# Optimization experiments

Hardware: AMD Instinct MI355X
Metric: run time of the kernel (lower is better)

Reference implementation:

```python
import jax, jax.numpy as jnp
import numpy as np

VOCAB, T, IN, H, L = 32000, 4096, 512, 256, 2


def setup_inputs() -> dict:
    key = jax.random.key(0)
    ks = jax.random.split(key, 32)
    inp = {}
    inp["tokens"] = jax.random.randint(ks[0], (T,), 0, VOCAB)
    inp["emb"] = jax.random.normal(ks[1], (VOCAB, IN), dtype=jnp.float32) * 0.02
    i = 2
    for d in ("f", "b"):
        for l in range(L):
            in_l = IN if l == 0 else H
            inp[f"{d}_Wih{l}"] = jax.random.normal(ks[i], (4 * H, in_l), dtype=jnp.float32) * 0.05; i += 1
            inp[f"{d}_Whh{l}"] = jax.random.normal(ks[i], (4 * H, H), dtype=jnp.float32) * 0.05; i += 1
            inp[f"{d}_bih{l}"] = jnp.zeros((4 * H,), dtype=jnp.float32)
            inp[f"{d}_bhh{l}"] = jnp.zeros((4 * H,), dtype=jnp.float32)
    return inp


def _lstm_layer(x_seq, Wih, Whh, bih, bhh):
    # x_seq: [T, in]; torch.nn.LSTMCell gate order: i, f, g, o
    Hh = Whh.shape[1]
    b = bih + bhh
    def step(carry, x):
        h, c = carry
        g = x @ Wih.T + h @ Whh.T + b           # [4H]
        i_, f_, g_, o_ = jnp.split(g, 4)
        c = jax.nn.sigmoid(f_) * c + jax.nn.sigmoid(i_) * jnp.tanh(g_)
        h = jax.nn.sigmoid(o_) * jnp.tanh(c)
        return (h, c), h
    z = jnp.zeros((Hh,), x_seq.dtype)
    (h, c), hs = jax.lax.scan(step, (z, z), x_seq)
    return hs, h, c                              # [T,H], [H], [H]


def _run_dir(x_seq, params):
    finals = []
    h_seq = x_seq
    for (Wih, Whh, bih, bhh) in params:
        h_seq, h, c = _lstm_layer(h_seq, Wih, Whh, bih, bhh)
        finals.append((c, h))
    return h_seq, finals


def reference(tokens, emb,
              f_Wih0, f_Whh0, f_bih0, f_bhh0, f_Wih1, f_Whh1, f_bih1, f_bhh1,
              b_Wih0, b_Whh0, b_bih0, b_bhh0, b_Wih1, b_Whh1, b_bih1, b_bhh1):
    x = emb[tokens]                              # [T, IN] embedding lookup
    fparams = [(f_Wih0, f_Whh0, f_bih0, f_bhh0), (f_Wih1, f_Whh1, f_bih1, f_bhh1)]
    bparams = [(b_Wih0, b_Whh0, b_bih0, b_bhh0), (b_Wih1, b_Whh1, b_bih1, b_bhh1)]
    f_out, f_fin = _run_dir(x, fparams)          # forward over sequence
    b_out_rev, b_fin = _run_dir(x[::-1], bparams)  # backward over reversed sequence
    b_out = b_out_rev[::-1]
    outputs = jnp.concatenate([f_out, b_out], axis=-1)  # [T, 2H]
    cell_memories = jnp.stack([jnp.stack([f_fin[l][0], b_fin[l][0]]) for l in range(L)])  # [L,2,H]
    hidden_states = jnp.stack([jnp.stack([f_fin[l][1], b_fin[l][1]]) for l in range(L)])  # [L,2,H]
    return cell_memories, hidden_states, outputs
```

## Files before the change

### kernel.cpp

```cpp
#include <hip/hip_runtime.h>
#include <math.h>

#define T_SEQ 4096

__device__ __forceinline__ float sigmoidf_(float x) {
  return 1.0f / (1.0f + expf(-x));
}

__device__ __forceinline__ unsigned long long pack_h(int tag, float h) {
  return ((unsigned long long)(unsigned)tag << 32) |
         (unsigned long long)__float_as_uint(h);
}

__device__ __forceinline__ unsigned long long ld_mall(const unsigned long long* p) {
  unsigned long long v;
  asm volatile("global_load_dwordx2 %0, %1, off sc0 sc1\n\ts_waitcnt vmcnt(0)"
               : "=v"(v) : "v"(p) : "memory");
  return v;
}
__device__ __forceinline__ void st_mall(unsigned long long* p, unsigned long long v) {
  asm volatile("global_store_dwordx2 %0, %1, off sc0 sc1"
               :: "v"(p), "v"(v) : "memory");
}
__device__ __forceinline__ float poll_mall(const unsigned long long* p, unsigned want) {
  for (;;) {
    unsigned long long v = ld_mall(p);
    if ((unsigned)(v >> 32) == want) return __uint_as_float((unsigned)v);
  }
}

__device__ __forceinline__ void bar() {
  asm volatile("s_waitcnt lgkmcnt(0)" ::: "memory");
  __builtin_amdgcn_s_barrier();
  asm volatile("" ::: "memory");
}

#define DECL_W8(p) float4 p##0, p##1, p##2, p##3, p##4, p##5, p##6, p##7
#define LOAD_W8(p, src) do { const float4* _s = (const float4*)(src); \
  p##0=_s[0]; p##1=_s[1]; p##2=_s[2]; p##3=_s[3]; \
  p##4=_s[4]; p##5=_s[5]; p##6=_s[6]; p##7=_s[7]; } while (0)
#define PIN4(v4) asm volatile("" : "+v"((v4).x), "+v"((v4).y), \
                                   "+v"((v4).z), "+v"((v4).w))
#define PIN_W8(p) do { PIN4(p##0); PIN4(p##1); PIN4(p##2); PIN4(p##3); \
  PIN4(p##4); PIN4(p##5); PIN4(p##6); PIN4(p##7); } while (0)
#define FMA4(acc, W_, H_) do { acc = fmaf((W_).x, (H_).x, acc); \
  acc = fmaf((W_).y, (H_).y, acc); acc = fmaf((W_).z, (H_).z, acc); \
  acc = fmaf((W_).w, (H_).w, acc); } while (0)

__global__ void gather_emb(const int* __restrict__ tokens,
                           const float4* __restrict__ emb4,
                           float4* __restrict__ X4) {
  int i = blockIdx.x * 256 + threadIdx.x;
  int t = i >> 7;
  int q = i & 127;
  X4[i] = emb4[(long)tokens[t] * 128 + q];
}

__global__ __launch_bounds__(256) void gemm_proj(
    const float* __restrict__ Xf, const float* __restrict__ Xb, int revb,
    const float* __restrict__ Wf, const float* __restrict__ Wb,
    const float* __restrict__ bihf, const float* __restrict__ bhhf,
    const float* __restrict__ bihb, const float* __restrict__ bhhb,
    float* __restrict__ Pf, float* __restrict__ Pb, int K)
{
  const int dirb = blockIdx.z;
  const float* X  = dirb ? Xb : Xf;
  const float* W  = dirb ? Wb : Wf;
  const float* bih = dirb ? bihb : bihf;
  const float* bhh = dirb ? bhhb : bhhf;
  float* Pp = dirb ? Pb : Pf;
  const int rev = dirb ? revb : 0;

  const int bn = blockIdx.x;
  const int bm = blockIdx.y;
  const int tid = threadIdx.x;
  const int tx = tid & 15, ty = tid >> 4;

  __shared__ float Xs[16][68];
  __shared__ float Ws[16][68];

  float acc[4][4] = {{0.f}};

  const int lrow = tid >> 2;
  const int lk4  = (tid & 3) * 4;
  const int xrow = bm * 64 + lrow;
  const int xsrc = rev ? (4095 - xrow) : xrow;
  const float* xptr = X + (long)xsrc * K + lk4;
  const float* wptr = W + (long)(bn * 64 + lrow) * K + lk4;

  for (int k0 = 0; k0 < K; k0 += 16) {
    float4 xv = *(const float4*)(xptr + k0);
    float4 wv = *(const float4*)(wptr + k0);
    __syncthreads();
    Xs[lk4 + 0][lrow] = xv.x; Xs[lk4 + 1][lrow] = xv.y;
    Xs[lk4 + 2][lrow] = xv.z; Xs[lk4 + 3][lrow] = xv.w;
    Ws[lk4 + 0][lrow] = wv.x; Ws[lk4 + 1][lrow] = wv.y;
    Ws[lk4 + 2][lrow] = wv.z; Ws[lk4 + 3][lrow] = wv.w;
    __syncthreads();
    #pragma unroll
    for (int kk = 0; kk < 16; ++kk) {
      float4 a = *(const float4*)(&Xs[kk][ty * 4]);
      float4 b = *(const float4*)(&Ws[kk][tx * 4]);
      acc[0][0] = fmaf(a.x, b.x, acc[0][0]); acc[0][1] = fmaf(a.x, b.y, acc[0][1]);
      acc[0][2] = fmaf(a.x, b.z, acc[0][2]); acc[0][3] = fmaf(a.x, b.w, acc[0][3]);
      acc[1][0] = fmaf(a.y, b.x, acc[1][0]); acc[1][1] = fmaf(a.y, b.y, acc[1][1]);
      acc[1][2] = fmaf(a.y, b.z, acc[1][2]); acc[1][3] = fmaf(a.y, b.w, acc[1][3]);
      acc[2][0] = fmaf(a.z, b.x, acc[2][0]); acc[2][1] = fmaf(a.z, b.y, acc[2][1]);
      acc[2][2] = fmaf(a.z, b.z, acc[2][2]); acc[2][3] = fmaf(a.z, b.w, acc[2][3]);
      acc[3][0] = fmaf(a.w, b.x, acc[3][0]); acc[3][1] = fmaf(a.w, b.y, acc[3][1]);
      acc[3][2] = fmaf(a.w, b.z, acc[3][2]); acc[3][3] = fmaf(a.w, b.w, acc[3][3]);
    }
  }

  const int c0 = bn * 64 + tx * 4;
  #pragma unroll
  for (int i = 0; i < 4; ++i) {
    const int r = bm * 64 + ty * 4 + i;
    float4 o4;
    o4.x = acc[i][0] + bih[c0 + 0] + bhh[c0 + 0];
    o4.y = acc[i][1] + bih[c0 + 1] + bhh[c0 + 1];
    o4.z = acc[i][2] + bih[c0 + 2] + bhh[c0 + 2];
    o4.w = acc[i][3] + bih[c0 + 3] + bhh[c0 + 3];
    *(float4*)(&Pp[(long)r * 1024 + c0]) = o4;
  }
}

__global__ __launch_bounds__(512, 1) void lstm_fused(
    const float* __restrict__ P0f, const float* __restrict__ P0b,
    const float* __restrict__ Whh0f, const float* __restrict__ Whh0b,
    const float* __restrict__ Wih1f, const float* __restrict__ Whh1f,
    const float* __restrict__ bih1f, const float* __restrict__ bhh1f,
    const float* __restrict__ Wih1b, const float* __restrict__ Whh1b,
    const float* __restrict__ bih1b, const float* __restrict__ bhh1b,
    float* __restrict__ out,
    unsigned long long* __restrict__ ring0,
    unsigned long long* __restrict__ h1x)
{
  const int bx = blockIdx.x;
  const int t  = threadIdx.x;
  const int d   = bx & 1;
  const int sub = bx >> 1;

  __shared__ float hx[512];
  __shared__ float part[8 * 264];

  unsigned long long* ring = ring0 + (long)d * T_SEQ * 256;

  if (sub < 4) {
    const int w = sub;
    const int wbase = w * 64;
    const float* __restrict__ P = d ? P0b : P0f;
    const float* __restrict__ W = d ? Whh0b : Whh0f;

    const int kb = t >> 6;
    const int jg = t & 63;

    DECL_W8(wa); DECL_W8(wb); DECL_W8(wc); DECL_W8(wd);
    LOAD_W8(wa, W + (long)(0 * 256 + wbase + jg) * 256 + kb * 32);
    LOAD_W8(wb, W + (long)(1 * 256 + wbase + jg) * 256 + kb * 32);
    LOAD_W8(wc, W + (long)(2 * 256 + wbase + jg) * 256 + kb * 32);
    LOAD_W8(wd, W + (long)(3 * 256 + wbase + jg) * 256 + kb * 32);
    PIN_W8(wa); PIN_W8(wb); PIN_W8(wc); PIN_W8(wd);

    const long pj = (long)((t & 3) * 256 + wbase + (t >> 2));

    float pv_cur = 0.0f, c_prev = 0.0f;
    if (t < 256) { pv_cur = P[pj]; hx[t] = 0.0f; }

    for (int s = 0; s < T_SEQ; ++s) {
      if (s > 0 && t >= 256 && t < 448) {
        const int q = t - 256;
        const int pcell = (q < wbase) ? q : q + 64;
        hx[pcell] = poll_mall(ring + (long)(s - 1) * 256 + pcell, (unsigned)s);
      }
      float pv_next = 0.0f;
      if (t < 256 && s + 1 < T_SEQ) pv_next = P[(long)(s + 1) * 1024 + pj];
      bar();

      float a0 = 0.f, a1 = 0.f, a2 = 0.f, a3 = 0.f;
      const float4* h4 = (const float4*)&hx[kb * 32];
      #define L0STEP(q) do { float4 hv = h4[q]; FMA4(a0, wa##q, hv); \
        FMA4(a1, wb##q, hv); FMA4(a2, wc##q, hv); FMA4(a3, wd##q, hv); } while (0)
      L0STEP(0); L0STEP(1); L0STEP(2); L0STEP(3);
      L0STEP(4); L0STEP(5); L0STEP(6); L0STEP(7);
      #undef L0STEP
      float4 av; av.x = a0; av.y = a1; av.z = a2; av.w = a3;
      *(float4*)(&part[kb * 264 + jg * 4]) = av;
      bar();

      if (t < 256) {
        float g = pv_cur;
        #pragma unroll
        for (int q = 0; q < 8; ++q) g += part[q * 264 + t];
        float act = ((t & 3) == 2) ? tanhf(g) : sigmoidf_(g);
        float y  = __shfl_xor(act, 1);
        float zx = __shfl_xor(act, 2);
        float zy = __shfl_xor(y, 2);
        const bool l1b = (t & 1), h1b = (t & 2);
        float i_ = h1b ? (l1b ? zy : zx) : (l1b ? y : act);
        float f_ = h1b ? (l1b ? zx : zy) : (l1b ? act : y);
        float g_ = h1b ? (l1b ? y : act) : (l1b ? zy : zx);
        float o_ = h1b ? (l1b ? act : y) : (l1b ? zx : zy);
        float c = f_ * c_prev + i_ * g_;
        c_prev = c;
        float h = o_ * tanhf(c);
        pv_cur = pv_next;
        if ((t & 3) == 0) {
          const int gc = wbase + (t >> 2);
          hx[gc] = h;
          st_mall(ring + (long)s * 256 + gc, pack_h(s + 1, h));
          if (s == T_SEQ - 1) {
            out[d * 256 + gc] = c;
            out[1024 + d * 256 + gc] = h;
          }
        }
      }
    }
  } else {
    const int w1 = sub - 4;
    const int wbase1 = w1 * 32;
    const float* __restrict__ Wih = d ? Wih1b : Wih1f;
    const float* __restrict__ Whh = d ? Whh1b : Whh1f;
    const float* __restrict__ bih = d ? bih1b : bih1f;
    const float* __restrict__ bhh = d ? bhh1b : bhh1f;
    unsigned long long* slot = h1x + d * 512;
    float* hout = d ? (out + 2048 + (long)4095 * 512 + 256) : (out + 2048);
    const long hstr = d ? -512 : 512;

    const int kb = t >> 6;
    const int jg = t & 63;

    const int m0 = jg * 2, m1 = m0 + 1;
    const int j0 = (m0 & 3) * 256 + wbase1 + (m0 >> 2);
    const int j1 = (m1 & 3) * 256 + wbase1 + (m1 >> 2);
    const float* s0 = (kb < 4) ? (Wih + (long)j0 * 256 + kb * 64)
                               : (Whh + (long)j0 * 256 + (kb - 4) * 64);
    const float* s1 = (kb < 4) ? (Wih + (long)j1 * 256 + kb * 64)
                               : (Whh + (long)j1 * 256 + (kb - 4) * 64);
    DECL_W8(ua); DECL_W8(ub); DECL_W8(uc); DECL_W8(ud);
    LOAD_W8(ua, s0); LOAD_W8(ub, s0 + 32);
    LOAD_W8(uc, s1); LOAD_W8(ud, s1 + 32);
    PIN_W8(ua); PIN_W8(ub); PIN_W8(uc); PIN_W8(ud);

    float bsum = 0.0f, c_prev = 0.0f;
    if (t < 128) {
      const int j = (t & 3) * 256 + wbase1 + (t >> 2);
      bsum = bih[j] + bhh[j];
      if ((t & 3) == 0) hx[256 + wbase1 + (t >> 2)] = 0.0f;
    }

    for (int s = 0; s < T_SEQ; ++s) {
      if (t >= 128 && t < 384) {
        const int c0_ = t - 128;
        hx[c0_] = poll_mall(ring + (long)s * 256 + c0_, (unsigned)(s + 1));
      } else {
        int q1 = -1;
        if (t < 128) { if ((t & 3) != 0) q1 = (t >> 2) * 3 + (t & 3) - 1; }
        else q1 = 96 + (t - 384);
        if (q1 >= 0) {
          const int pc1 = (q1 < wbase1) ? q1 : q1 + 32;
          hx[256 + pc1] = poll_mall(slot + ((s + 1) & 1) * 256 + pc1,
                                    (unsigned)s);
        }
      }
      bar();

      float a0 = 0.f, a1 = 0.f;
      const float4* h4 = (const float4*)&hx[kb * 64];
      #define L1STEPA(q) do { float4 hv = h4[q];     FMA4(a0, ua##q, hv); \
        FMA4(a1, uc##q, hv); } while (0)
      #define L1STEPB(q) do { float4 hv = h4[8 + q]; FMA4(a0, ub##q, hv); \
        FMA4(a1, ud##q, hv); } while (0)
      L1STEPA(0); L1STEPA(1); L1STEPA(2); L1STEPA(3);
      L1STEPA(4); L1STEPA(5); L1STEPA(6); L1STEPA(7);
      L1STEPB(0); L1STEPB(1); L1STEPB(2); L1STEPB(3);
      L1STEPB(4); L1STEPB(5); L1STEPB(6); L1STEPB(7);
      #undef L1STEPA
      #undef L1STEPB
      float2 av2; av2.x = a0; av2.y = a1;
      *(float2*)(&part[kb * 264 + jg * 2]) = av2;
      bar();

      if (t < 128) {
        float g = bsum;
        #pragma unroll
        for (int q = 0; q < 8; ++q) g += part[q * 264 + t];
        float act = ((t & 3) == 2) ? tanhf(g) : sigmoidf_(g);
        float y  = __shfl_xor(act, 1);
        float zx = __shfl_xor(act, 2);
        float zy = __shfl_xor(y, 2);
        const bool l1b = (t & 1), h1b = (t & 2);
        float i_ = h1b ? (l1b ? zy : zx) : (l1b ? y : act);
        float f_ = h1b ? (l1b ? zx : zy) : (l1b ? act : y);
        float g_ = h1b ? (l1b ? y : act) : (l1b ? zy : zx);
        float o_ = h1b ? (l1b ? act : y) : (l1b ? zx : zy);
        float c = f_ * c_prev + i_ * g_;
        c_prev = c;
        float h = o_ * tanhf(c);
        if ((t & 3) == 0) {
          const int gc = wbase1 + (t >> 2);
          hx[256 + gc] = h;
          st_mall(&slot[(s & 1) * 256 + gc], pack_h(s + 1, h));
          hout[(long)s * hstr + gc] = h;
          if (s == T_SEQ - 1) {
            out[512 + d * 256 + gc] = c;
            out[1024 + 512 + d * 256 + gc] = h;
          }
        }
      }
    }
  }
}

extern "C" void kernel_launch(void* const* d_in, const int* in_sizes, int n_in,
                              void* d_out, int out_size, void* d_ws, size_t ws_size,
                              hipStream_t stream) {
  const int*   tokens = (const int*)d_in[0];
  const float* emb    = (const float*)d_in[1];
  const float* fWih0 = (const float*)d_in[2];
  const float* fWhh0 = (const float*)d_in[3];
  const float* fbih0 = (const float*)d_in[4];
  const float* fbhh0 = (const float*)d_in[5];
  const float* fWih1 = (const float*)d_in[6];
  const float* fWhh1 = (const float*)d_in[7];
  const float* fbih1 = (const float*)d_in[8];
  const float* fbhh1 = (const float*)d_in[9];
  const float* bWih0 = (const float*)d_in[10];
  const float* bWhh0 = (const float*)d_in[11];
  const float* bbih0 = (const float*)d_in[12];
  const float* bbhh0 = (const float*)d_in[13];
  const float* bWih1 = (const float*)d_in[14];
  const float* bWhh1 = (const float*)d_in[15];
  const float* bbih1 = (const float*)d_in[16];
  const float* bbhh1 = (const float*)d_in[17];

  float* out = (float*)d_out;
  float* ws  = (float*)d_ws;

  float* X   = ws;
  float* P0f = ws + 4194304;
  float* P0b = ws + 8388608;
  unsigned long long* ring0 = (unsigned long long*)ws;
  unsigned long long* h1x   = (unsigned long long*)(ws + 12582912);

  gather_emb<<<2048, 256, 0, stream>>>(tokens, (const float4*)emb, (float4*)X);

  gemm_proj<<<dim3(16, 64, 2), 256, 0, stream>>>(
      X, X, 1, fWih0, bWih0, fbih0, fbhh0, bbih0, bbhh0, P0f, P0b, 512);

  hipMemsetAsync(ring0, 0, (size_t)2 * T_SEQ * 256 * sizeof(unsigned long long), stream);
  hipMemsetAsync(h1x, 0, 1024 * sizeof(unsigned long long), stream);

  lstm_fused<<<dim3(24), 512, 0, stream>>>(
      P0f, P0b, fWhh0, bWhh0,
      fWih1, fWhh1, fbih1, fbhh1,
      bWih1, bWhh1, bbih1, bbhh1,
      out, ring0, h1x);
}
```

Measured before the change: 7.064 ms.

## Replace LDS partial-sum reduction with lane shuffles and double-buffer hidden state

Remaps the threads of each recurrent block so that the lanes sharing one gate row split the K dimension, and combines their partial dot products with xor shuffles instead of writing them to shared memory. This removes the second barrier per timestep. The hidden-state buffer is double-buffered in shared memory so that the next step's writes cannot race with the current step's reads. Cross-block flag loads and stores switch from cache-bypassing inline asm to atomicOr and atomicExch, which may raise the latency of each poll.

Result: slower. 12.16 ms (+72.2%).

```diff
diff --git a/kernel.cpp b/kernel.cpp
--- a/kernel.cpp
+++ b/kernel.cpp
@@ -12,19 +12,12 @@
          (unsigned long long)__float_as_uint(h);
 }
 
-__device__ __forceinline__ unsigned long long ld_mall(const unsigned long long* p) {
-  unsigned long long v;
-  asm volatile("global_load_dwordx2 %0, %1, off sc0 sc1\n\ts_waitcnt vmcnt(0)"
-               : "=v"(v) : "v"(p) : "memory");
-  return v;
-}
-__device__ __forceinline__ void st_mall(unsigned long long* p, unsigned long long v) {
-  asm volatile("global_store_dwordx2 %0, %1, off sc0 sc1"
-               :: "v"(p), "v"(v) : "memory");
-}
-__device__ __forceinline__ float poll_mall(const unsigned long long* p, unsigned want) {
+__device__ __forceinline__ void st_a(unsigned long long* p, unsigned long long v) {
+  atomicExch(p, v);
+}
+__device__ __forceinline__ float poll_a(unsigned long long* p, unsigned want) {
   for (;;) {
-    unsigned long long v = ld_mall(p);
+    unsigned long long v = atomicOr(p, 0ull);
     if ((unsigned)(v >> 32) == want) return __uint_as_float((unsigned)v);
   }
 }
@@ -46,6 +39,16 @@
 #define FMA4(acc, W_, H_) do { acc = fmaf((W_).x, (H_).x, acc); \
   acc = fmaf((W_).y, (H_).y, acc); acc = fmaf((W_).z, (H_).z, acc); \
   acc = fmaf((W_).w, (H_).w, acc); } while (0)
+#define G8(acc, p, off) do { \
+  { float4 hv = h4[off + 0]; FMA4(acc, p##0, hv); } \
+  { float4 hv = h4[off + 1]; FMA4(acc, p##1, hv); } \
+  { float4 hv = h4[off + 2]; FMA4(acc, p##2, hv); } \
+  { float4 hv = h4[off + 3]; FMA4(acc, p##3, hv); } \
+  { float4 hv = h4[off + 4]; FMA4(acc, p##4, hv); } \
+  { float4 hv = h4[off + 5]; FMA4(acc, p##5, hv); } \
+  { float4 hv = h4[off + 6]; FMA4(acc, p##6, hv); } \
+  { float4 hv = h4[off + 7]; FMA4(acc, p##7, hv); } \
+} while (0)
 
 __global__ void gather_emb(const int* __restrict__ tokens,
                            const float4* __restrict__ emb4,
@@ -141,8 +144,7 @@
   const int d   = bx & 1;
   const int sub = bx >> 1;
 
-  __shared__ float hx[512];
-  __shared__ float part[8 * 264];
+  __shared__ float hx2[2][512];
 
   unsigned long long* ring = ring0 + (long)d * T_SEQ * 256;
 
@@ -152,67 +154,55 @@
     const float* __restrict__ P = d ? P0b : P0f;
     const float* __restrict__ W = d ? Whh0b : Whh0f;
 
-    const int kb = t >> 6;
-    const int jg = t & 63;
+    const int cell = t >> 3, gate = (t >> 1) & 3, kh = t & 1;
+    const int j = gate * 256 + wbase + cell;
 
     DECL_W8(wa); DECL_W8(wb); DECL_W8(wc); DECL_W8(wd);
-    LOAD_W8(wa, W + (long)(0 * 256 + wbase + jg) * 256 + kb * 32);
-    LOAD_W8(wb, W + (long)(1 * 256 + wbase + jg) * 256 + kb * 32);
-    LOAD_W8(wc, W + (long)(2 * 256 + wbase + jg) * 256 + kb * 32);
-    LOAD_W8(wd, W + (long)(3 * 256 + wbase + jg) * 256 + kb * 32);
+    const float* wsrc = W + (long)j * 256 + kh * 128;
+    LOAD_W8(wa, wsrc); LOAD_W8(wb, wsrc + 32);
+    LOAD_W8(wc, wsrc + 64); LOAD_W8(wd, wsrc + 96);
     PIN_W8(wa); PIN_W8(wb); PIN_W8(wc); PIN_W8(wd);
 
-    const long pj = (long)((t & 3) * 256 + wbase + (t >> 2));
-
-    float pv_cur = 0.0f, c_prev = 0.0f;
-    if (t < 256) { pv_cur = P[pj]; hx[t] = 0.0f; }
+    float pv_cur = P[j];
+    float c_prev = 0.0f;
+    if (t < 256) hx2[0][t] = 0.0f;
 
     for (int s = 0; s < T_SEQ; ++s) {
-      if (s > 0 && t >= 256 && t < 448) {
-        const int q = t - 256;
-        const int pcell = (q < wbase) ? q : q + 64;
-        hx[pcell] = poll_mall(ring + (long)(s - 1) * 256 + pcell, (unsigned)s);
+      if (s > 0 && t < 192) {
+        const int pcell = (t < wbase) ? t : t + 64;
+        hx2[s & 1][pcell] = poll_a(ring + (long)(s - 1) * 256 + pcell,
+                                   (unsigned)s);
       }
       float pv_next = 0.0f;
-      if (t < 256 && s + 1 < T_SEQ) pv_next = P[(long)(s + 1) * 1024 + pj];
+      if (s + 1 < T_SEQ) pv_next = P[(long)(s + 1) * 1024 + j];
       bar();
 
+      const float4* h4 = (const float4*)&hx2[s & 1][kh * 128];
       float a0 = 0.f, a1 = 0.f, a2 = 0.f, a3 = 0.f;
-      const float4* h4 = (const float4*)&hx[kb * 32];
-      #define L0STEP(q) do { float4 hv = h4[q]; FMA4(a0, wa##q, hv); \
-        FMA4(a1, wb##q, hv); FMA4(a2, wc##q, hv); FMA4(a3, wd##q, hv); } while (0)
-      L0STEP(0); L0STEP(1); L0STEP(2); L0STEP(3);
-      L0STEP(4); L0STEP(5); L0STEP(6); L0STEP(7);
-      #undef L0STEP
-      float4 av; av.x = a0; av.y = a1; av.z = a2; av.w = a3;
-      *(float4*)(&part[kb * 264 + jg * 4]) = av;
-      bar();
-
-      if (t < 256) {
-        float g = pv_cur;
-        #pragma unroll
-        for (int q = 0; q < 8; ++q) g += part[q * 264 + t];
-        float act = ((t & 3) == 2) ? tanhf(g) : sigmoidf_(g);
-        float y  = __shfl_xor(act, 1);
-        float zx = __shfl_xor(act, 2);
-        float zy = __shfl_xor(y, 2);
-        const bool l1b = (t & 1), h1b = (t & 2);
-        float i_ = h1b ? (l1b ? zy : zx) : (l1b ? y : act);
-        float f_ = h1b ? (l1b ? zx : zy) : (l1b ? act : y);
-        float g_ = h1b ? (l1b ? y : act) : (l1b ? zy : zx);
-        float o_ = h1b ? (l1b ? act : y) : (l1b ? zx : zy);
-        float c = f_ * c_prev + i_ * g_;
-        c_prev = c;
-        float h = o_ * tanhf(c);
-        pv_cur = pv_next;
-        if ((t & 3) == 0) {
-          const int gc = wbase + (t >> 2);
-          hx[gc] = h;
-          st_mall(ring + (long)s * 256 + gc, pack_h(s + 1, h));
-          if (s == T_SEQ - 1) {
-            out[d * 256 + gc] = c;
-            out[1024 + d * 256 + gc] = h;
-          }
+      G8(a0, wa, 0); G8(a1, wb, 8); G8(a2, wc, 16); G8(a3, wd, 24);
+      float sum = (a0 + a1) + (a2 + a3);
+      float tot = sum + __shfl_xor(sum, 1);
+      float g = pv_cur + tot;
+      pv_cur = pv_next;
+      float act = ((t & 6) == 4) ? tanhf(g) : sigmoidf_(g);
+      float y  = __shfl_xor(act, 2);
+      float zx = __shfl_xor(act, 4);
+      float zy = __shfl_xor(y, 4);
+      const bool l1b = (t & 2), h1b = (t & 4);
+      float i_ = h1b ? (l1b ? zy : zx) : (l1b ? y : act);
+      float f_ = h1b ? (l1b ? zx : zy) : (l1b ? act : y);
+      float g_ = h1b ? (l1b ? y : act) : (l1b ? zy : zx);
+      float o_ = h1b ? (l1b ? act : y) : (l1b ? zx : zy);
+      float c = f_ * c_prev + i_ * g_;
+      c_prev = c;
+      float h = o_ * tanhf(c);
+      if ((t & 7) == 0) {
+        const int gc = wbase + cell;
+        hx2[(s + 1) & 1][gc] = h;
+        st_a(ring + (long)s * 256 + gc, pack_h(s + 1, h));
+        if (s == T_SEQ - 1) {
+          out[d * 256 + gc] = c;
+          out[1024 + d * 256 + gc] = h;
         }
       }
     }
@@ -227,85 +217,58 @@
     float* hout = d ? (out + 2048 + (long)4095 * 512 + 256) : (out + 2048);
     const long hstr = d ? -512 : 512;
 
-    const int kb = t >> 6;
-    const int jg = t & 63;
-
-    const int m0 = jg * 2, m1 = m0 + 1;
-    const int j0 = (m0 & 3) * 256 + wbase1 + (m0 >> 2);
-    const int j1 = (m1 & 3) * 256 + wbase1 + (m1 >> 2);
-    const float* s0 = (kb < 4) ? (Wih + (long)j0 * 256 + kb * 64)
-                               : (Whh + (long)j0 * 256 + (kb - 4) * 64);
-    const float* s1 = (kb < 4) ? (Wih + (long)j1 * 256 + kb * 64)
-                               : (Whh + (long)j1 * 256 + (kb - 4) * 64);
+    const int cell = t >> 4, gate = (t >> 2) & 3, kq = t & 3;
+    const int j = gate * 256 + wbase1 + cell;
+
     DECL_W8(ua); DECL_W8(ub); DECL_W8(uc); DECL_W8(ud);
-    LOAD_W8(ua, s0); LOAD_W8(ub, s0 + 32);
-    LOAD_W8(uc, s1); LOAD_W8(ud, s1 + 32);
+    const float* usrc = (kq < 2) ? (Wih + (long)j * 256 + kq * 128)
+                                 : (Whh + (long)j * 256 + (kq - 2) * 128);
+    LOAD_W8(ua, usrc); LOAD_W8(ub, usrc + 32);
+    LOAD_W8(uc, usrc + 64); LOAD_W8(ud, usrc + 96);
     PIN_W8(ua); PIN_W8(ub); PIN_W8(uc); PIN_W8(ud);
 
-    float bsum = 0.0f, c_prev = 0.0f;
-    if (t < 128) {
-      const int j = (t & 3) * 256 + wbase1 + (t >> 2);
-      bsum = bih[j] + bhh[j];
-      if ((t & 3) == 0) hx[256 + wbase1 + (t >> 2)] = 0.0f;
-    }
+    const float bsum = bih[j] + bhh[j];
+    float c_prev = 0.0f;
+    if ((t & 15) == 0) hx2[0][256 + wbase1 + cell] = 0.0f;
 
     for (int s = 0; s < T_SEQ; ++s) {
-      if (t >= 128 && t < 384) {
-        const int c0_ = t - 128;
-        hx[c0_] = poll_mall(ring + (long)s * 256 + c0_, (unsigned)(s + 1));
-      } else {
-        int q1 = -1;
-        if (t < 128) { if ((t & 3) != 0) q1 = (t >> 2) * 3 + (t & 3) - 1; }
-        else q1 = 96 + (t - 384);
-        if (q1 >= 0) {
-          const int pc1 = (q1 < wbase1) ? q1 : q1 + 32;
-          hx[256 + pc1] = poll_mall(slot + ((s + 1) & 1) * 256 + pc1,
-                                    (unsigned)s);
-        }
+      if (t < 256) {
+        hx2[s & 1][t] = poll_a(ring + (long)s * 256 + t, (unsigned)(s + 1));
+      } else if (t < 480) {
+        const int q1 = t - 256;
+        const int pc1 = (q1 < wbase1) ? q1 : q1 + 32;
+        hx2[s & 1][256 + pc1] =
+            poll_a(slot + ((s + 1) & 1) * 256 + pc1, (unsigned)s);
       }
       bar();
 
-      float a0 = 0.f, a1 = 0.f;
-      const float4* h4 = (const float4*)&hx[kb * 64];
-      #define L1STEPA(q) do { float4 hv = h4[q];     FMA4(a0, ua##q, hv); \
-        FMA4(a1, uc##q, hv); } while (0)
-      #define L1STEPB(q) do { float4 hv = h4[8 + q]; FMA4(a0, ub##q, hv); \
-        FMA4(a1, ud##q, hv); } while (0)
-      L1STEPA(0); L1STEPA(1); L1STEPA(2); L1STEPA(3);
-      L1STEPA(4); L1STEPA(5); L1STEPA(6); L1STEPA(7);
-      L1STEPB(0); L1STEPB(1); L1STEPB(2); L1STEPB(3);
-      L1STEPB(4); L1STEPB(5); L1STEPB(6); L1STEPB(7);
-      #undef L1STEPA
-      #undef L1STEPB
-      float2 av2; av2.x = a0; av2.y = a1;
-      *(float2*)(&part[kb * 264 + jg * 2]) = av2;
-      bar();
-
-      if (t < 128) {
-        float g = bsum;
-        #pragma unroll
-        for (int q = 0; q < 8; ++q) g += part[q * 264 + t];
-        float act = ((t & 3) == 2) ? tanhf(g) : sigmoidf_(g);
-        float y  = __shfl_xor(act, 1);
-        float zx = __shfl_xor(act, 2);
-        float zy = __shfl_xor(y, 2);
-        const bool l1b = (t & 1), h1b = (t & 2);
-        float i_ = h1b ? (l1b ? zy : zx) : (l1b ? y : act);
-        float f_ = h1b ? (l1b ? zx : zy) : (l1b ? act : y);
-        float g_ = h1b ? (l1b ? y : act) : (l1b ? zy : zx);
-        float o_ = h1b ? (l1b ? act : y) : (l1b ? zx : zy);
-        float c = f_ * c_prev + i_ * g_;
-        c_prev = c;
-        float h = o_ * tanhf(c);
-        if ((t & 3) == 0) {
-          const int gc = wbase1 + (t >> 2);
-          hx[256 + gc] = h;
-          st_mall(&slot[(s & 1) * 256 + gc], pack_h(s + 1, h));
-          hout[(long)s * hstr + gc] = h;
-          if (s == T_SEQ - 1) {
-            out[512 + d * 256 + gc] = c;
-            out[1024 + 512 + d * 256 + gc] = h;
-          }
+      const float4* h4 = (const float4*)&hx2[s & 1][kq * 128];
+      float a0 = 0.f, a1 = 0.f, a2 = 0.f, a3 = 0.f;
+      G8(a0, ua, 0); G8(a1, ub, 8); G8(a2, uc, 16); G8(a3, ud, 24);
+      float sum = (a0 + a1) + (a2 + a3);
+      float r1 = sum + __shfl_xor(sum, 1);
+      float r2 = r1 + __shfl_xor(r1, 2);
+      float g = bsum + r2;
+      float act = ((t & 12) == 8) ? tanhf(g) : sigmoidf_(g);
+      float y  = __shfl_xor(act, 4);
+      float zx = __shfl_xor(act, 8);
+      float zy = __shfl_xor(y, 8);
+      const bool l1b = (t & 4), h1b = (t & 8);
+      float i_ = h1b ? (l1b ? zy : zx) : (l1b ? y : act);
+      float f_ = h1b ? (l1b ? zx : zy) : (l1b ? act : y);
+      float g_ = h1b ? (l1b ? y : act) : (l1b ? zy : zx);
+      float o_ = h1b ? (l1b ? act : y) : (l1b ? zx : zy);
+      float c = f_ * c_prev + i_ * g_;
+      c_prev = c;
+      float h = o_ * tanhf(c);
+      if ((t & 15) == 0) {
+        const int gc = wbase1 + cell;
+        hx2[(s + 1) & 1][256 + gc] = h;
+        st_a(&slot[(s & 1) * 256 + gc], pack_h(s + 1, h));
+        hout[(long)s * hstr + gc] = h;
+        if (s == T_SEQ - 1) {
+          out[512 + d * 256 + gc] = c;
+          out[1024 + 512 + d * 256 + gc] = h;
         }
       }
     }
```
